# Kernel optimization log

Hardware: AMD Instinct MI355X
Metric: run time of the kernel (lower is better)

## Reference

```python
import jax, jax.numpy as jnp
import numpy as np


def setup_inputs() -> dict:
    key = jax.random.key(0)
    k1, k2, k3 = jax.random.split(key, 3)
    N, E, D = 100000, 3200000, 32  # neurons, total edges (fan-in sum), feature dim
    src = jax.random.normal(k1, (N, D), dtype=jnp.float32)
    gather_idx = jax.random.randint(k2, (E,), 0, N, dtype=jnp.int32)
    # repeat_interleave(arange(N), repeats) is nondecreasing -> sorted segment ids
    segment_ids = jnp.sort(jax.random.randint(k3, (E,), 0, N, dtype=jnp.int32))
    return {"src": src, "gather_idx": gather_idx, "segment_ids": segment_ids, "num_segments": N}


def reference(src, gather_idx, segment_ids, num_segments):
    # gather neuron input values: [E, D]
    gathered = src[gather_idx]
    # scatter_mean over variable-length groups (segment mean)
    sums = jax.ops.segment_sum(gathered, segment_ids, num_segments=num_segments,
                               indices_are_sorted=True)
    counts = jax.ops.segment_sum(jnp.ones((gathered.shape[0],), dtype=src.dtype),
                                 segment_ids, num_segments=num_segments,
                                 indices_are_sorted=True)
    return sums / jnp.maximum(counts, 1.0)[:, None]
```

## Files before the change

kernel.cpp:

```cpp
#include <hip/hip_runtime.h>


constexpr int D = 32;
constexpr int GSZ = 8;
constexpr int BLOCK = 256;
constexpr int SEGS_PER_BLOCK = BLOCK / GSZ;

__device__ __forceinline__ int lower_bound_i32(const int* __restrict__ a, int lo, int hi, int key) {
    while (lo < hi) {
        int mid = (lo + hi) >> 1;
        int v = a[mid];
        if (v < key) lo = mid + 1;
        else         hi = mid;
    }
    return lo;
}

__global__ __launch_bounds__(BLOCK) void AggregationLayer_53051436040325_kernel(
    const float* __restrict__ src,
    const int*   __restrict__ gidx,
    const int*   __restrict__ segid,
    float*       __restrict__ out,
    int E, int N)
{
    const int n   = blockIdx.x * SEGS_PER_BLOCK + (threadIdx.x >> 3);
    const int sub = threadIdx.x & (GSZ - 1);
    if (n >= N) return;

    const int lo = lower_bound_i32(segid, 0, E, n);
    const int hi = lower_bound_i32(segid, lo, E, n + 1);

    const float* srcp = src + (size_t)sub * 4;

    float4 acc = make_float4(0.f, 0.f, 0.f, 0.f);
    int e = lo;
    for (; e + 4 <= hi; e += 4) {
        const int g0 = gidx[e + 0];
        const int g1 = gidx[e + 1];
        const int g2 = gidx[e + 2];
        const int g3 = gidx[e + 3];
        const float4 v0 = *(const float4*)(srcp + (size_t)g0 * D);
        const float4 v1 = *(const float4*)(srcp + (size_t)g1 * D);
        const float4 v2 = *(const float4*)(srcp + (size_t)g2 * D);
        const float4 v3 = *(const float4*)(srcp + (size_t)g3 * D);
        acc.x += (v0.x + v1.x) + (v2.x + v3.x);
        acc.y += (v0.y + v1.y) + (v2.y + v3.y);
        acc.z += (v0.z + v1.z) + (v2.z + v3.z);
        acc.w += (v0.w + v1.w) + (v2.w + v3.w);
    }
    for (; e < hi; ++e) {
        const int g = gidx[e];
        const float4 v = *(const float4*)(srcp + (size_t)g * D);
        acc.x += v.x; acc.y += v.y; acc.z += v.z; acc.w += v.w;
    }

    const int c = hi - lo;
    const float cnt = (float)(c > 0 ? c : 1);
    float4 r;
    r.x = acc.x / cnt;
    r.y = acc.y / cnt;
    r.z = acc.z / cnt;
    r.w = acc.w / cnt;
    *(float4*)(out + (size_t)n * D + sub * 4) = r;
}

extern "C" void kernel_launch(void* const* d_in, const int* in_sizes, int n_in,
                              void* d_out, int out_size, void* d_ws, size_t ws_size,
                              hipStream_t stream) {
    const float* src   = (const float*)d_in[0];
    const int*   gidx  = (const int*)d_in[1];
    const int*   segid = (const int*)d_in[2];
    const int E = in_sizes[1];
    const int N = in_sizes[0] / D;

    float* out = (float*)d_out;
    const int blocks = (N + SEGS_PER_BLOCK - 1) / SEGS_PER_BLOCK;
    AggregationLayer_53051436040325_kernel<<<blocks, BLOCK, 0, stream>>>(src, gidx, segid, out, E, N);
}
```

Measured before the change: 154.0 us.

## Precompute segment offsets in a boundary kernel and unroll gather loop by eight

Adds a first kernel that scans the sorted segment ids once and writes a CSR-style start offset array into workspace. The aggregation kernel then reads start[n] and start[n+1] instead of doing two binary searches over the full edge array for each neuron. The gather loop is also widened from four to eight outstanding row loads per iteration to raise memory-level parallelism. In exchange it adds a second launch, a full pass over segid, and a dependency on a workspace buffer of N+1 ints.

```diff
diff --git a/kernel.cpp b/kernel.cpp
--- a/kernel.cpp
+++ b/kernel.cpp
@@ -6,47 +6,48 @@
 constexpr int BLOCK = 256;
 constexpr int SEGS_PER_BLOCK = BLOCK / GSZ;
 
-__device__ __forceinline__ int lower_bound_i32(const int* __restrict__ a, int lo, int hi, int key) {
-    while (lo < hi) {
-        int mid = (lo + hi) >> 1;
-        int v = a[mid];
-        if (v < key) lo = mid + 1;
-        else         hi = mid;
-    }
-    return lo;
+__global__ __launch_bounds__(BLOCK) void seg_bounds_kernel(
+    const int* __restrict__ segid,
+    int*       __restrict__ start,
+    int E, int N)
+{
+    int e = blockIdx.x * BLOCK + threadIdx.x;
+    if (e > E) return;
+    int s, p;
+    if (e == E) { s = N; p = segid[E - 1]; }
+    else        { s = segid[e]; p = (e == 0) ? -1 : segid[e - 1]; }
+    for (int n = p + 1; n <= s; ++n) start[n] = e;
 }
 
 __global__ __launch_bounds__(BLOCK) void AggregationLayer_53051436040325_kernel(
     const float* __restrict__ src,
     const int*   __restrict__ gidx,
-    const int*   __restrict__ segid,
+    const int*   __restrict__ start,
     float*       __restrict__ out,
-    int E, int N)
+    int N)
 {
     const int n   = blockIdx.x * SEGS_PER_BLOCK + (threadIdx.x >> 3);
     const int sub = threadIdx.x & (GSZ - 1);
     if (n >= N) return;
 
-    const int lo = lower_bound_i32(segid, 0, E, n);
-    const int hi = lower_bound_i32(segid, lo, E, n + 1);
+    const int lo = start[n];
+    const int hi = start[n + 1];
 
     const float* srcp = src + (size_t)sub * 4;
 
     float4 acc = make_float4(0.f, 0.f, 0.f, 0.f);
     int e = lo;
-    for (; e + 4 <= hi; e += 4) {
-        const int g0 = gidx[e + 0];
-        const int g1 = gidx[e + 1];
-        const int g2 = gidx[e + 2];
-        const int g3 = gidx[e + 3];
-        const float4 v0 = *(const float4*)(srcp + (size_t)g0 * D);
-        const float4 v1 = *(const float4*)(srcp + (size_t)g1 * D);
-        const float4 v2 = *(const float4*)(srcp + (size_t)g2 * D);
-        const float4 v3 = *(const float4*)(srcp + (size_t)g3 * D);
-        acc.x += (v0.x + v1.x) + (v2.x + v3.x);
-        acc.y += (v0.y + v1.y) + (v2.y + v3.y);
-        acc.z += (v0.z + v1.z) + (v2.z + v3.z);
-        acc.w += (v0.w + v1.w) + (v2.w + v3.w);
+    for (; e + 8 <= hi; e += 8) {
+        int g[8];
+#pragma unroll
+        for (int j = 0; j < 8; ++j) g[j] = gidx[e + j];
+        float4 v[8];
+#pragma unroll
+        for (int j = 0; j < 8; ++j) v[j] = *(const float4*)(srcp + (size_t)g[j] * D);
+#pragma unroll
+        for (int j = 0; j < 8; ++j) {
+            acc.x += v[j].x; acc.y += v[j].y; acc.z += v[j].z; acc.w += v[j].w;
+        }
     }
     for (; e < hi; ++e) {
         const int g = gidx[e];
@@ -73,7 +74,12 @@
     const int E = in_sizes[1];
     const int N = in_sizes[0] / D;
 
-    float* out = (float*)d_out;
-    const int blocks = (N + SEGS_PER_BLOCK - 1) / SEGS_PER_BLOCK;
-    AggregationLayer_53051436040325_kernel<<<blocks, BLOCK, 0, stream>>>(src, gidx, segid, out, E, N);
+    int*   start = (int*)d_ws;
+    float* out   = (float*)d_out;
+
+    const int blocksA = (E + 1 + BLOCK - 1) / BLOCK;
+    seg_bounds_kernel<<<blocksA, BLOCK, 0, stream>>>(segid, start, E, N);
+
+    const int blocksB = (N + SEGS_PER_BLOCK - 1) / SEGS_PER_BLOCK;
+    AggregationLayer_53051436040325_kernel<<<blocksB, BLOCK, 0, stream>>>(src, gidx, start, out, N);
 }
```

Result: faster. 136.3 us (-11.5%).
